# Kernel optimization log

Hardware: AMD Instinct MI355X
Metric: run time of the kernel (lower is better)

## Reference

```python
import jax, jax.numpy as jnp
import numpy as np

B, T, V = 2, 2048, 256
C, H, L = 1024, 16, 8
DH = C // H  # 64


def setup_inputs() -> dict:
    key = jax.random.key(0)
    ks = jax.random.split(key, 12)
    s = 0.02
    return {
        "x": jax.random.normal(ks[0], (B, T, V), jnp.float32),
        "W_emb": jax.random.normal(ks[1], (V, C), jnp.float32) * s,
        "b_emb": jnp.zeros((C,), jnp.float32),
        "pos": jax.random.normal(ks[2], (1, T, C), jnp.float32) * s,
        "Wqkv": jax.random.normal(ks[3], (L, C, 3 * C), jnp.float32) * s,
        "bqkv": jnp.zeros((L, 3 * C), jnp.float32),
        "Wproj": jax.random.normal(ks[4], (L, C, C), jnp.float32) * s,
        "bproj": jnp.zeros((L, C), jnp.float32),
        "gamma": jnp.ones((C,), jnp.float32),
        "beta": jnp.zeros((C,), jnp.float32),
        "W_out": jax.random.normal(ks[5], (C, V), jnp.float32) * s,
        "b_out": jnp.zeros((V,), jnp.float32),
    }


def _attn_block(h, Wqkv_l, bqkv_l, Wproj_l, bproj_l):
    # h: [B, T, C]
    qkv = h @ Wqkv_l + bqkv_l                      # [B, T, 3C]
    q, k, v = jnp.split(qkv, 3, axis=-1)
    q = q.reshape(B, T, H, DH)
    k = k.reshape(B, T, H, DH)
    v = v.reshape(B, T, H, DH)
    scale = 1.0 / np.sqrt(DH).astype(np.float32)
    att = jnp.einsum("bthd,bshd->bhts", q, k) * scale   # [B, H, T, T]
    att = jax.nn.softmax(att, axis=-1)
    y = jnp.einsum("bhts,bshd->bthd", att, v)            # [B, T, H, DH]
    y = y.reshape(B, T, C)
    return y @ Wproj_l + bproj_l


def reference(x, W_emb, b_emb, pos, Wqkv, bqkv, Wproj, bproj, gamma, beta, W_out, b_out):
    h = x @ W_emb + b_emb            # dense embedding: Linear(V -> C)
    h = h + pos[:, :T, :]
    # NOTE: original blocks return attention output directly (no residual, no MLP)
    def body(h, params):
        Wq, bq, Wp, bp = params
        return _attn_block(h, Wq, bq, Wp, bp), None
    h, _ = jax.lax.scan(body, h, (Wqkv, bqkv, Wproj, bproj))
    # LayerNorm
    mu = jnp.mean(h, axis=-1, keepdims=True)
    var = jnp.mean(jnp.square(h - mu), axis=-1, keepdims=True)
    h = (h - mu) * jax.lax.rsqrt(var + 1e-5) * gamma + beta
    return h @ W_out + b_out          # [B, T, V]
```

## Files before the change

kernel.cpp:

```cpp
#include <hip/hip_runtime.h>
#include <hip/hip_bf16.h>

#define T_SEQ 2048
#define BATCH 2
#define CDIM 1024
#define VDIM 256
#define NHEAD 16
#define DHEAD 64
#define NLAYER 8
#define MROWS (BATCH * T_SEQ)

typedef __attribute__((ext_vector_type(8))) short bf16x8;
typedef __attribute__((ext_vector_type(4))) float f32x4;
typedef __attribute__((ext_vector_type(4))) int i32x4;

#define SELHI 0x07060302u
#define SELLO 0x05040100u
#define QSCALE 0.18033688011112042f

__device__ __forceinline__ uint prm(uint a, uint b, uint s) { return __builtin_amdgcn_perm(a, b, s); }

__device__ __forceinline__ uint bf16rne(float f) {
    uint u = __float_as_uint(f);
    return (u + 0x7fffu + ((u >> 16) & 1u)) & 0xffff0000u;
}
__device__ __forceinline__ uint packsplit(float x) {
    uint hb = bf16rne(x);
    float d = x - __uint_as_float(hb);
    uint lb = bf16rne(d);
    return prm(hb, lb, SELHI);
}
__device__ __forceinline__ float unpack2(uint u) {
    return __uint_as_float(u & 0xffff0000u) + __uint_as_float(u << 16);
}
__device__ __forceinline__ bf16x8 asb(i32x4 v) {
    union { i32x4 i; bf16x8 b; } u; u.i = v; return u.b;
}
__device__ __forceinline__ short bfs(float f) { return (short)(bf16rne(f) >> 16); }


__global__ __launch_bounds__(256) void gemm_f32_kernel(
    const float* __restrict__ A, const float* __restrict__ B,
    const float* __restrict__ bias, const float* __restrict__ addrow,
    float* __restrict__ C, int M, int N, int K, int addmod, int out_mode)
{
    __shared__ float As[16][64];
    __shared__ float Bs[16][68];

    const int tid = threadIdx.x;
    const int bn = blockIdx.x * 64;
    const int bm = blockIdx.y * 64;

    const int lrow = tid >> 2;
    const int lkq  = (tid & 3) * 4;
    const int lkr  = tid >> 4;
    const int lnq  = (tid & 15) * 4;
    const int ty   = tid >> 4;
    const int tx   = tid & 15;

    float acc[4][4];
#pragma unroll
    for (int i = 0; i < 4; ++i)
#pragma unroll
        for (int j = 0; j < 4; ++j) acc[i][j] = 0.f;

    for (int k0 = 0; k0 < K; k0 += 16) {
        __syncthreads();
        {
            float4 a4 = *(const float4*)&A[(size_t)(bm + lrow) * K + k0 + lkq];
            As[lkq + 0][lrow] = a4.x;
            As[lkq + 1][lrow] = a4.y;
            As[lkq + 2][lrow] = a4.z;
            As[lkq + 3][lrow] = a4.w;
            *(float4*)&Bs[lkr][lnq] =
                *(const float4*)&B[(size_t)(k0 + lkr) * N + bn + lnq];
        }
        __syncthreads();
#pragma unroll
        for (int kk = 0; kk < 16; ++kk) {
            const float4 a = *(const float4*)&As[kk][ty * 4];
            const float4 b = *(const float4*)&Bs[kk][tx * 4];
            acc[0][0] += a.x * b.x; acc[0][1] += a.x * b.y; acc[0][2] += a.x * b.z; acc[0][3] += a.x * b.w;
            acc[1][0] += a.y * b.x; acc[1][1] += a.y * b.y; acc[1][2] += a.y * b.z; acc[1][3] += a.y * b.w;
            acc[2][0] += a.z * b.x; acc[2][1] += a.z * b.y; acc[2][2] += a.z * b.z; acc[2][3] += a.z * b.w;
            acc[3][0] += a.w * b.x; acc[3][1] += a.w * b.y; acc[3][2] += a.w * b.z; acc[3][3] += a.w * b.w;
        }
    }

    const int ncol = bn + tx * 4;
    const float4 bv = *(const float4*)&bias[ncol];
#pragma unroll
    for (int i = 0; i < 4; ++i) {
        const int mrow = bm + ty * 4 + i;
        float4 o;
        o.x = acc[i][0] + bv.x;
        o.y = acc[i][1] + bv.y;
        o.z = acc[i][2] + bv.z;
        o.w = acc[i][3] + bv.w;
        if (addrow) {
            const float4 p = *(const float4*)&addrow[(size_t)(mrow % addmod) * N + ncol];
            o.x += p.x; o.y += p.y; o.z += p.z; o.w += p.w;
        }
        if (out_mode == 0) {
            *(float4*)&C[(size_t)mrow * N + ncol] = o;
        } else {
            const size_t addr = ((size_t)(mrow >> 4) * (N >> 5) + (ncol >> 5)) * 512
                              + (size_t)(((ncol >> 2) & 3) * 16 + (mrow & 15)) * 8
                              + 4 * ((ncol >> 4) & 1);
            uint4 pk;
            pk.x = packsplit(o.x); pk.y = packsplit(o.y);
            pk.z = packsplit(o.z); pk.w = packsplit(o.w);
            *(uint4*)&((uint*)C)[addr] = pk;
        }
    }
}

__global__ __launch_bounds__(256) void wsplit_kernel(
    const float* __restrict__ W, short* __restrict__ Fh, short* __restrict__ Fl,
    int N, int K)
{
    const int ln = threadIdx.x & 63, lk = threadIdx.x >> 6;
    const int n  = blockIdx.x * 64 + ln;
    const int kq = blockIdx.y * 4 + lk;
    const int k0 = kq * 4;

    float f0 = W[(size_t)(k0 + 0) * N + n];
    float f1 = W[(size_t)(k0 + 1) * N + n];
    float f2 = W[(size_t)(k0 + 2) * N + n];
    float f3 = W[(size_t)(k0 + 3) * N + n];
    uint h0 = bf16rne(f0), h1 = bf16rne(f1), h2 = bf16rne(f2), h3 = bf16rne(f3);
    uint l0 = bf16rne(f0 - __uint_as_float(h0));
    uint l1 = bf16rne(f1 - __uint_as_float(h1));
    uint l2 = bf16rne(f2 - __uint_as_float(h2));
    uint l3 = bf16rne(f3 - __uint_as_float(h3));

    const int gl = kq & 3, j0 = ((kq >> 2) & 1) * 4;
    const size_t base = (((size_t)(n >> 4) * (K >> 5) + (kq >> 3)) * 64 + gl * 16 + (n & 15)) * 8 + j0;
    *(int2*)&Fh[base] = make_int2((int)prm(h1, h0, SELHI), (int)prm(h3, h2, SELHI));
    *(int2*)&Fl[base] = make_int2((int)prm(l1, l0, SELHI), (int)prm(l3, l2, SELHI));
}

template <int TERMS>
__global__ __launch_bounds__(256) void gemm_mfma_kernel(
    const uint* __restrict__ Apf, const short* __restrict__ Bhf,
    const short* __restrict__ Blf, const float* __restrict__ bias,
    uint* __restrict__ Cv, uint* __restrict__ Cq, short* __restrict__ Ckf,
    short* __restrict__ Cvf, int M, int N, int K, int out_mode)
{
    const int tid = threadIdx.x, lane = tid & 63, w = tid >> 6;
    const int wr = w >> 1, wc = w & 1, x = lane & 15, gl = lane >> 4;
    const int bm = blockIdx.y * 128, bn = blockIdx.x * 128;
    const int nkc = K >> 5;

    const uint*  ab = Apf + ((size_t)((bm >> 4) + wr * 4) * nkc) * 512 + (size_t)lane * 8;
    const short* hb = Bhf + (((size_t)((bn >> 4) + wc * 4) * nkc) * 64 + lane) * 8;
    const short* lb = Blf + (((size_t)((bn >> 4) + wc * 4) * nkc) * 64 + lane) * 8;
    const size_t tstr = (size_t)nkc * 512;

    f32x4 acc[4][4];
#pragma unroll
    for (int mi = 0; mi < 4; ++mi)
#pragma unroll
        for (int ni = 0; ni < 4; ++ni) acc[mi][ni] = (f32x4){0.f, 0.f, 0.f, 0.f};

    for (int kc = 0; kc < nkc; ++kc) {
        const size_t ko = (size_t)kc * 512;
        bf16x8 ah[4], al[4], bh[4], bl[4];
#pragma unroll
        for (int t = 0; t < 4; ++t) {
            const uint* ap = ab + t * tstr + ko;
            uint4 a0 = *(const uint4*)ap;
            uint4 a1 = *(const uint4*)(ap + 4);
            i32x4 h4;
            h4[0] = (int)prm(a0.y, a0.x, SELHI); h4[1] = (int)prm(a0.w, a0.z, SELHI);
            h4[2] = (int)prm(a1.y, a1.x, SELHI); h4[3] = (int)prm(a1.w, a1.z, SELHI);
            ah[t] = asb(h4);
            if (TERMS >= 2) {
                i32x4 l4;
                l4[0] = (int)prm(a0.y, a0.x, SELLO); l4[1] = (int)prm(a0.w, a0.z, SELLO);
                l4[2] = (int)prm(a1.y, a1.x, SELLO); l4[3] = (int)prm(a1.w, a1.z, SELLO);
                al[t] = asb(l4);
            }
            bh[t] = *(const bf16x8*)(hb + t * tstr + ko);
            if (TERMS >= 3) bl[t] = *(const bf16x8*)(lb + t * tstr + ko);
        }
        __builtin_amdgcn_s_setprio(1);
#pragma unroll
        for (int mi = 0; mi < 4; ++mi)
#pragma unroll
            for (int ni = 0; ni < 4; ++ni) {
                acc[mi][ni] = __builtin_amdgcn_mfma_f32_16x16x32_bf16(ah[mi], bh[ni], acc[mi][ni], 0, 0, 0);
                if (TERMS >= 3)
                    acc[mi][ni] = __builtin_amdgcn_mfma_f32_16x16x32_bf16(ah[mi], bl[ni], acc[mi][ni], 0, 0, 0);
                if (TERMS >= 2)
                    acc[mi][ni] = __builtin_amdgcn_mfma_f32_16x16x32_bf16(al[mi], bh[ni], acc[mi][ni], 0, 0, 0);
            }
        __builtin_amdgcn_s_setprio(0);
    }

#pragma unroll
    for (int ni = 0; ni < 4; ++ni) {
        const int n = bn + wc * 64 + ni * 16 + x;
        const float bv = bias[n];
#pragma unroll
        for (int mi = 0; mi < 4; ++mi) {
            const int m0 = bm + wr * 64 + mi * 16 + gl * 4;
            const f32x4 o = acc[mi][ni];
            if (out_mode == 2) {
                const size_t mt = (size_t)(bm >> 4) + wr * 4 + mi;
                const size_t base = (mt * (N >> 5) + (n >> 5)) * 512
                                  + (size_t)(((n >> 2) & 3) * 16 + gl * 4) * 8
                                  + (n & 3) + 4 * ((n >> 4) & 1);
                Cv[base + 0 * 8] = packsplit(o[0] + bv);
                Cv[base + 1 * 8] = packsplit(o[1] + bv);
                Cv[base + 2 * 8] = packsplit(o[2] + bv);
                Cv[base + 3 * 8] = packsplit(o[3] + bv);
            } else if (n < 1024) {
                Cq[(size_t)(m0 + 0) * 1024 + n] = packsplit((o[0] + bv) * QSCALE);
                Cq[(size_t)(m0 + 1) * 1024 + n] = packsplit((o[1] + bv) * QSCALE);
                Cq[(size_t)(m0 + 2) * 1024 + n] = packsplit((o[2] + bv) * QSCALE);
                Cq[(size_t)(m0 + 3) * 1024 + n] = packsplit((o[3] + bv) * QSCALE);
            } else if (n < 2048) {
                const int dd6 = n - 1024;
                const int hhh = dd6 >> 6, ch = (dd6 >> 5) & 1, dd = dd6 & 31;
                const int bq = m0 >> 11, sv = m0 & (T_SEQ - 1);
                const size_t base = ((((size_t)(bq * NHEAD + hhh) * 128 + (sv >> 4)) * 2 + ch) * 64
                                    + 16 * ((dd & 15) >> 2) + (sv & 15)) * 8
                                    + (dd & 3) + 4 * (dd >> 4);
                Ckf[base + 0]  = bfs(o[0] + bv);
                Ckf[base + 8]  = bfs(o[1] + bv);
                Ckf[base + 16] = bfs(o[2] + bv);
                Ckf[base + 24] = bfs(o[3] + bv);
            } else {
                const int dd6 = n - 2048;
                const int hhh = dd6 >> 6, dmi = (dd6 >> 4) & 3, xt = dd6 & 15;
                const int bq = m0 >> 11, sv = m0 & (T_SEQ - 1);
                const size_t base = ((((size_t)(bq * NHEAD + hhh) * 64 + (sv >> 5)) * 4 + dmi) * 64
                                    + xt + 16 * ((sv & 15) >> 2)) * 8 + 4 * ((sv >> 4) & 1);
                short4 st;
                st.x = bfs(o[0] + bv); st.y = bfs(o[1] + bv);
                st.z = bfs(o[2] + bv); st.w = bfs(o[3] + bv);
                *(short4*)&Cvf[base] = st;
            }
        }
    }
}

__global__ __launch_bounds__(256) void attn_mfma_kernel(
    const uint* __restrict__ qrow, const short* __restrict__ kf,
    const short* __restrict__ vf, uint* __restrict__ y)
{
    const int tid  = threadIdx.x;
    const int w    = tid >> 6;
    const int lane = tid & 63;
    const int x    = lane & 15;
    const int gl   = lane >> 4;

    const int orig = blockIdx.x;
    const int wgid = (orig & 7) * 64 + (orig >> 3);
    const int bh = wgid >> 4;
    const int b = bh >> 4, hh = bh & 15;
    const int t0 = (wgid & 15) * 128;

    i32x4 qhi[2][2];
#pragma unroll
    for (int qf = 0; qf < 2; ++qf) {
        const uint* qp = qrow + (size_t)(b * T_SEQ + t0 + 64 * qf + 16 * w + x) * 1024 + hh * 64;
#pragma unroll
        for (int ch = 0; ch < 2; ++ch) {
            uint4 a0 = *(const uint4*)(qp + 32 * ch + 4 * gl);
            uint4 a1 = *(const uint4*)(qp + 32 * ch + 16 + 4 * gl);
            qhi[qf][ch][0] = (int)prm(a0.y, a0.x, SELHI); qhi[qf][ch][1] = (int)prm(a0.w, a0.z, SELHI);
            qhi[qf][ch][2] = (int)prm(a1.y, a1.x, SELHI); qhi[qf][ch][3] = (int)prm(a1.w, a1.z, SELHI);
        }
    }

    const short* kb = kf + (size_t)bh * 128 * 2 * 512 + (size_t)lane * 8;
    const short* vb = vf + (size_t)bh * 64 * 4 * 512 + (size_t)lane * 8;

    i32x4 ones4;
    ones4[0] = ones4[1] = ones4[2] = ones4[3] = 0x3F803F80;

    f32x4 oacc[2][4], lacc[2];
#pragma unroll
    for (int qf = 0; qf < 2; ++qf) {
        lacc[qf] = (f32x4){0.f, 0.f, 0.f, 0.f};
#pragma unroll
        for (int i = 0; i < 4; ++i) oacc[qf][i] = (f32x4){0.f, 0.f, 0.f, 0.f};
    }

    for (int s0 = 0; s0 < T_SEQ; s0 += 64) {
        bf16x8 kh[4][2], vh[2][4];
#pragma unroll
        for (int sc = 0; sc < 4; ++sc)
#pragma unroll
            for (int ch = 0; ch < 2; ++ch)
                kh[sc][ch] = *(const bf16x8*)(kb + ((((size_t)(s0 >> 4) + sc) * 2 + ch) * 512));
#pragma unroll
        for (int ch = 0; ch < 2; ++ch)
#pragma unroll
            for (int dm = 0; dm < 4; ++dm)
                vh[ch][dm] = *(const bf16x8*)(vb + ((((size_t)(s0 >> 5) + ch) * 4 + dm) * 512));

#pragma unroll
        for (int qf = 0; qf < 2; ++qf) {
            f32x4 s4[4];
#pragma unroll
            for (int sc = 0; sc < 4; ++sc) {
                s4[sc] = (f32x4){0.f, 0.f, 0.f, 0.f};
                s4[sc] = __builtin_amdgcn_mfma_f32_16x16x32_bf16(kh[sc][0], asb(qhi[qf][0]), s4[sc], 0, 0, 0);
                s4[sc] = __builtin_amdgcn_mfma_f32_16x16x32_bf16(kh[sc][1], asb(qhi[qf][1]), s4[sc], 0, 0, 0);
            }
#pragma unroll
            for (int sc = 0; sc < 4; ++sc) {
                s4[sc][0] = __builtin_amdgcn_exp2f(s4[sc][0]);
                s4[sc][1] = __builtin_amdgcn_exp2f(s4[sc][1]);
                s4[sc][2] = __builtin_amdgcn_exp2f(s4[sc][2]);
                s4[sc][3] = __builtin_amdgcn_exp2f(s4[sc][3]);
            }
            i32x4 pfh[2];
#pragma unroll
            for (int c = 0; c < 2; ++c) {
                f32x4 pa = s4[2 * c], pb = s4[2 * c + 1];
                pfh[c][0] = (int)prm(__float_as_uint(pa[1]), __float_as_uint(pa[0]), SELHI);
                pfh[c][1] = (int)prm(__float_as_uint(pa[3]), __float_as_uint(pa[2]), SELHI);
                pfh[c][2] = (int)prm(__float_as_uint(pb[1]), __float_as_uint(pb[0]), SELHI);
                pfh[c][3] = (int)prm(__float_as_uint(pb[3]), __float_as_uint(pb[2]), SELHI);
            }
            lacc[qf] = __builtin_amdgcn_mfma_f32_16x16x32_bf16(asb(ones4), asb(pfh[0]), lacc[qf], 0, 0, 0);
            lacc[qf] = __builtin_amdgcn_mfma_f32_16x16x32_bf16(asb(ones4), asb(pfh[1]), lacc[qf], 0, 0, 0);
#pragma unroll
            for (int dm = 0; dm < 4; ++dm) {
                oacc[qf][dm] = __builtin_amdgcn_mfma_f32_16x16x32_bf16(vh[0][dm], asb(pfh[0]), oacc[qf][dm], 0, 0, 0);
                oacc[qf][dm] = __builtin_amdgcn_mfma_f32_16x16x32_bf16(vh[1][dm], asb(pfh[1]), oacc[qf][dm], 0, 0, 0);
            }
        }
    }

#pragma unroll
    for (int qf = 0; qf < 2; ++qf) {
        const float invl = 1.f / lacc[qf][0];
        const size_t mt = (size_t)((b * T_SEQ + t0) >> 4) + 4 * qf + w;
#pragma unroll
        for (int dm = 0; dm < 4; ++dm) {
            f32x4 o = oacc[qf][dm];
            const size_t addr = (mt * 32 + hh * 2 + (dm >> 1)) * 512
                              + (size_t)lane * 8 + 4 * (dm & 1);
            uint4 pk;
            pk.x = packsplit(o[0] * invl); pk.y = packsplit(o[1] * invl);
            pk.z = packsplit(o[2] * invl); pk.w = packsplit(o[3] * invl);
            *(uint4*)&y[addr] = pk;
        }
    }
}

__global__ __launch_bounds__(256) void ln_kernel(
    const uint* __restrict__ h, const float* __restrict__ gamma,
    const float* __restrict__ beta, float* __restrict__ out)
{
    const int row = blockIdx.x;
    const int tid = threadIdx.x;

    const size_t addr = ((size_t)(row >> 4) * 32 + (tid >> 3)) * 512
                      + (size_t)((tid & 3) * 16 + (row & 15)) * 8
                      + 4 * ((tid >> 2) & 1);
    uint4 u = *(const uint4*)&h[addr];
    float4 v;
    v.x = unpack2(u.x); v.y = unpack2(u.y); v.z = unpack2(u.z); v.w = unpack2(u.w);

    float s  = v.x + v.y + v.z + v.w;
    float ss = v.x * v.x + v.y * v.y + v.z * v.z + v.w * v.w;
#pragma unroll
    for (int off = 1; off < 64; off <<= 1) {
        s  += __shfl_xor(s, off);
        ss += __shfl_xor(ss, off);
    }
    __shared__ float rs[4], rss[4];
    const int wid = tid >> 6;
    if ((tid & 63) == 0) { rs[wid] = s; rss[wid] = ss; }
    __syncthreads();
    s  = rs[0] + rs[1] + rs[2] + rs[3];
    ss = rss[0] + rss[1] + rss[2] + rss[3];

    const float mu   = s * (1.f / (float)CDIM);
    const float var  = ss * (1.f / (float)CDIM) - mu * mu;
    const float rstd = rsqrtf(var + 1e-5f);

    const float4 g  = *(const float4*)&gamma[tid * 4];
    const float4 be = *(const float4*)&beta[tid * 4];
    float4 o;
    o.x = (v.x - mu) * rstd * g.x + be.x;
    o.y = (v.y - mu) * rstd * g.y + be.y;
    o.z = (v.z - mu) * rstd * g.z + be.z;
    o.w = (v.w - mu) * rstd * g.w + be.w;
    *(float4*)&out[(size_t)row * CDIM + tid * 4] = o;
}

extern "C" void kernel_launch(void* const* d_in, const int* in_sizes, int n_in,
                              void* d_out, int out_size, void* d_ws, size_t ws_size,
                              hipStream_t stream)
{
    const float* x      = (const float*)d_in[0];
    const float* W_emb  = (const float*)d_in[1];
    const float* b_emb  = (const float*)d_in[2];
    const float* pos    = (const float*)d_in[3];
    const float* Wqkv   = (const float*)d_in[4];
    const float* bqkv   = (const float*)d_in[5];
    const float* Wproj  = (const float*)d_in[6];
    const float* bproj  = (const float*)d_in[7];
    const float* gamma  = (const float*)d_in[8];
    const float* beta   = (const float*)d_in[9];
    const float* W_out  = (const float*)d_in[10];
    const float* b_out  = (const float*)d_in[11];
    float* out = (float*)d_out;

    uint* h    = (uint*)d_ws;
    uint* qrow = h + (size_t)MROWS * CDIM;
    uint* y    = qrow + (size_t)MROWS * CDIM;
    short* kf  = (short*)(y + (size_t)MROWS * CDIM);
    short* vfb = kf + (size_t)32 * 128 * 2 * 512;
    short* Bqh = vfb + (size_t)32 * 64 * 4 * 512;
    short* Bql = Bqh + (size_t)3 * CDIM * CDIM;
    short* Bph = Bql + (size_t)3 * CDIM * CDIM;
    short* Bpl = Bph + (size_t)CDIM * CDIM;

    const dim3 blk(256);
    const int nattn = (T_SEQ / 128) * BATCH * NHEAD;

    gemm_f32_kernel<<<dim3(CDIM / 64, MROWS / 64), blk, 0, stream>>>(
        x, W_emb, b_emb, pos, (float*)h, MROWS, CDIM, VDIM, T_SEQ, 2);
    for (int l = 0; l < NLAYER; ++l) {
        wsplit_kernel<<<dim3(3 * CDIM / 64, CDIM / 16), blk, 0, stream>>>(
            Wqkv + (size_t)l * CDIM * 3 * CDIM, Bqh, Bql, 3 * CDIM, CDIM);
        gemm_mfma_kernel<1><<<dim3(3 * CDIM / 128, MROWS / 128), blk, 0, stream>>>(
            h, Bqh, Bql, bqkv + (size_t)l * 3 * CDIM,
            nullptr, qrow, kf, vfb, MROWS, 3 * CDIM, CDIM, 3);
        attn_mfma_kernel<<<dim3(nattn), blk, 0, stream>>>(qrow, kf, vfb, y);
        wsplit_kernel<<<dim3(CDIM / 64, CDIM / 16), blk, 0, stream>>>(
            Wproj + (size_t)l * CDIM * CDIM, Bph, Bpl, CDIM, CDIM);
        gemm_mfma_kernel<3><<<dim3(CDIM / 128, MROWS / 128), blk, 0, stream>>>(
            y, Bph, Bpl, bproj + (size_t)l * CDIM,
            h, nullptr, nullptr, nullptr, MROWS, CDIM, CDIM, 2);
    }
    ln_kernel<<<dim3(MROWS), blk, 0, stream>>>(h, gamma, beta, (float*)y);
    gemm_f32_kernel<<<dim3(VDIM / 64, MROWS / 64), blk, 0, stream>>>(
        (float*)y, W_out, b_out, nullptr, out, MROWS, VDIM, CDIM, 1, 0);
}
```

Before: 1.191 ms.

## Move embedding and output projections onto split-bf16 MFMA GEMM path

Replaces the scalar fp32 GEMMs for the embedding and output projection with the split-bf16 MFMA GEMM. It adds packing kernels for x and the weights, fuses the positional add into the GEMM epilogue and makes LayerNorm emit the packed split format. It also skips computing and writing the unused low-part of Wqkv, since the QKV GEMM only uses one term. This adds extra pack/split launches and relies on the three-term bf16 split to keep fp32-level accuracy.

```diff
diff --git a/kernel.cpp b/kernel.cpp
--- a/kernel.cpp
+++ b/kernel.cpp
@@ -39,80 +39,20 @@
 __device__ __forceinline__ short bfs(float f) { return (short)(bf16rne(f) >> 16); }
 
 
-__global__ __launch_bounds__(256) void gemm_f32_kernel(
-    const float* __restrict__ A, const float* __restrict__ B,
-    const float* __restrict__ bias, const float* __restrict__ addrow,
-    float* __restrict__ C, int M, int N, int K, int addmod, int out_mode)
-{
-    __shared__ float As[16][64];
-    __shared__ float Bs[16][68];
-
-    const int tid = threadIdx.x;
-    const int bn = blockIdx.x * 64;
-    const int bm = blockIdx.y * 64;
-
-    const int lrow = tid >> 2;
-    const int lkq  = (tid & 3) * 4;
-    const int lkr  = tid >> 4;
-    const int lnq  = (tid & 15) * 4;
-    const int ty   = tid >> 4;
-    const int tx   = tid & 15;
-
-    float acc[4][4];
-#pragma unroll
-    for (int i = 0; i < 4; ++i)
-#pragma unroll
-        for (int j = 0; j < 4; ++j) acc[i][j] = 0.f;
-
-    for (int k0 = 0; k0 < K; k0 += 16) {
-        __syncthreads();
-        {
-            float4 a4 = *(const float4*)&A[(size_t)(bm + lrow) * K + k0 + lkq];
-            As[lkq + 0][lrow] = a4.x;
-            As[lkq + 1][lrow] = a4.y;
-            As[lkq + 2][lrow] = a4.z;
-            As[lkq + 3][lrow] = a4.w;
-            *(float4*)&Bs[lkr][lnq] =
-                *(const float4*)&B[(size_t)(k0 + lkr) * N + bn + lnq];
-        }
-        __syncthreads();
-#pragma unroll
-        for (int kk = 0; kk < 16; ++kk) {
-            const float4 a = *(const float4*)&As[kk][ty * 4];
-            const float4 b = *(const float4*)&Bs[kk][tx * 4];
-            acc[0][0] += a.x * b.x; acc[0][1] += a.x * b.y; acc[0][2] += a.x * b.z; acc[0][3] += a.x * b.w;
-            acc[1][0] += a.y * b.x; acc[1][1] += a.y * b.y; acc[1][2] += a.y * b.z; acc[1][3] += a.y * b.w;
-            acc[2][0] += a.z * b.x; acc[2][1] += a.z * b.y; acc[2][2] += a.z * b.z; acc[2][3] += a.z * b.w;
-            acc[3][0] += a.w * b.x; acc[3][1] += a.w * b.y; acc[3][2] += a.w * b.z; acc[3][3] += a.w * b.w;
-        }
-    }
-
-    const int ncol = bn + tx * 4;
-    const float4 bv = *(const float4*)&bias[ncol];
-#pragma unroll
-    for (int i = 0; i < 4; ++i) {
-        const int mrow = bm + ty * 4 + i;
-        float4 o;
-        o.x = acc[i][0] + bv.x;
-        o.y = acc[i][1] + bv.y;
-        o.z = acc[i][2] + bv.z;
-        o.w = acc[i][3] + bv.w;
-        if (addrow) {
-            const float4 p = *(const float4*)&addrow[(size_t)(mrow % addmod) * N + ncol];
-            o.x += p.x; o.y += p.y; o.z += p.z; o.w += p.w;
-        }
-        if (out_mode == 0) {
-            *(float4*)&C[(size_t)mrow * N + ncol] = o;
-        } else {
-            const size_t addr = ((size_t)(mrow >> 4) * (N >> 5) + (ncol >> 5)) * 512
-                              + (size_t)(((ncol >> 2) & 3) * 16 + (mrow & 15)) * 8
-                              + 4 * ((ncol >> 4) & 1);
-            uint4 pk;
-            pk.x = packsplit(o.x); pk.y = packsplit(o.y);
-            pk.z = packsplit(o.z); pk.w = packsplit(o.w);
-            *(uint4*)&((uint*)C)[addr] = pk;
-        }
-    }
+__global__ __launch_bounds__(256) void packx_kernel(
+    const float* __restrict__ x, uint* __restrict__ xpf)
+{
+    const int t  = blockIdx.x * 256 + threadIdx.x;
+    const int m  = t >> 6;
+    const int k0 = (t & 63) * 4;
+    const float4 v = *(const float4*)&x[(size_t)m * 256 + k0];
+    const size_t addr = ((size_t)(m >> 4) * 8 + (k0 >> 5)) * 512
+                      + (size_t)(((k0 >> 2) & 3) * 16 + (m & 15)) * 8
+                      + 4 * ((k0 >> 4) & 1);
+    uint4 pk;
+    pk.x = packsplit(v.x); pk.y = packsplit(v.y);
+    pk.z = packsplit(v.z); pk.w = packsplit(v.w);
+    *(uint4*)&xpf[addr] = pk;
 }
 
 __global__ __launch_bounds__(256) void wsplit_kernel(
@@ -129,21 +69,24 @@
     float f2 = W[(size_t)(k0 + 2) * N + n];
     float f3 = W[(size_t)(k0 + 3) * N + n];
     uint h0 = bf16rne(f0), h1 = bf16rne(f1), h2 = bf16rne(f2), h3 = bf16rne(f3);
-    uint l0 = bf16rne(f0 - __uint_as_float(h0));
-    uint l1 = bf16rne(f1 - __uint_as_float(h1));
-    uint l2 = bf16rne(f2 - __uint_as_float(h2));
-    uint l3 = bf16rne(f3 - __uint_as_float(h3));
 
     const int gl = kq & 3, j0 = ((kq >> 2) & 1) * 4;
     const size_t base = (((size_t)(n >> 4) * (K >> 5) + (kq >> 3)) * 64 + gl * 16 + (n & 15)) * 8 + j0;
     *(int2*)&Fh[base] = make_int2((int)prm(h1, h0, SELHI), (int)prm(h3, h2, SELHI));
-    *(int2*)&Fl[base] = make_int2((int)prm(l1, l0, SELHI), (int)prm(l3, l2, SELHI));
+    if (Fl) {
+        uint l0 = bf16rne(f0 - __uint_as_float(h0));
+        uint l1 = bf16rne(f1 - __uint_as_float(h1));
+        uint l2 = bf16rne(f2 - __uint_as_float(h2));
+        uint l3 = bf16rne(f3 - __uint_as_float(h3));
+        *(int2*)&Fl[base] = make_int2((int)prm(l1, l0, SELHI), (int)prm(l3, l2, SELHI));
+    }
 }
 
 template <int TERMS>
 __global__ __launch_bounds__(256) void gemm_mfma_kernel(
     const uint* __restrict__ Apf, const short* __restrict__ Bhf,
     const short* __restrict__ Blf, const float* __restrict__ bias,
+    const float* __restrict__ addrow,
     uint* __restrict__ Cv, uint* __restrict__ Cq, short* __restrict__ Ckf,
     short* __restrict__ Cvf, int M, int N, int K, int out_mode)
 {
@@ -206,15 +149,28 @@
         for (int mi = 0; mi < 4; ++mi) {
             const int m0 = bm + wr * 64 + mi * 16 + gl * 4;
             const f32x4 o = acc[mi][ni];
-            if (out_mode == 2) {
+            if (out_mode == 0) {
+                float* C = (float*)Cv;
+                C[(size_t)(m0 + 0) * N + n] = o[0] + bv;
+                C[(size_t)(m0 + 1) * N + n] = o[1] + bv;
+                C[(size_t)(m0 + 2) * N + n] = o[2] + bv;
+                C[(size_t)(m0 + 3) * N + n] = o[3] + bv;
+            } else if (out_mode == 2) {
+                float p0 = 0.f, p1 = 0.f, p2 = 0.f, p3 = 0.f;
+                if (addrow) {
+                    p0 = addrow[(size_t)((m0 + 0) & (T_SEQ - 1)) * N + n];
+                    p1 = addrow[(size_t)((m0 + 1) & (T_SEQ - 1)) * N + n];
+                    p2 = addrow[(size_t)((m0 + 2) & (T_SEQ - 1)) * N + n];
+                    p3 = addrow[(size_t)((m0 + 3) & (T_SEQ - 1)) * N + n];
+                }
                 const size_t mt = (size_t)(bm >> 4) + wr * 4 + mi;
                 const size_t base = (mt * (N >> 5) + (n >> 5)) * 512
                                   + (size_t)(((n >> 2) & 3) * 16 + gl * 4) * 8
                                   + (n & 3) + 4 * ((n >> 4) & 1);
-                Cv[base + 0 * 8] = packsplit(o[0] + bv);
-                Cv[base + 1 * 8] = packsplit(o[1] + bv);
-                Cv[base + 2 * 8] = packsplit(o[2] + bv);
-                Cv[base + 3 * 8] = packsplit(o[3] + bv);
+                Cv[base + 0 * 8] = packsplit(o[0] + bv + p0);
+                Cv[base + 1 * 8] = packsplit(o[1] + bv + p1);
+                Cv[base + 2 * 8] = packsplit(o[2] + bv + p2);
+                Cv[base + 3 * 8] = packsplit(o[3] + bv + p3);
             } else if (n < 1024) {
                 Cq[(size_t)(m0 + 0) * 1024 + n] = packsplit((o[0] + bv) * QSCALE);
                 Cq[(size_t)(m0 + 1) * 1024 + n] = packsplit((o[1] + bv) * QSCALE);
@@ -356,7 +312,7 @@
 
 __global__ __launch_bounds__(256) void ln_kernel(
     const uint* __restrict__ h, const float* __restrict__ gamma,
-    const float* __restrict__ beta, float* __restrict__ out)
+    const float* __restrict__ beta, uint* __restrict__ outp)
 {
     const int row = blockIdx.x;
     const int tid = threadIdx.x;
@@ -388,12 +344,12 @@
 
     const float4 g  = *(const float4*)&gamma[tid * 4];
     const float4 be = *(const float4*)&beta[tid * 4];
-    float4 o;
-    o.x = (v.x - mu) * rstd * g.x + be.x;
-    o.y = (v.y - mu) * rstd * g.y + be.y;
-    o.z = (v.z - mu) * rstd * g.z + be.z;
-    o.w = (v.w - mu) * rstd * g.w + be.w;
-    *(float4*)&out[(size_t)row * CDIM + tid * 4] = o;
+    uint4 pk;
+    pk.x = packsplit((v.x - mu) * rstd * g.x + be.x);
+    pk.y = packsplit((v.y - mu) * rstd * g.y + be.y);
+    pk.z = packsplit((v.z - mu) * rstd * g.z + be.z);
+    pk.w = packsplit((v.w - mu) * rstd * g.w + be.w);
+    *(uint4*)&outp[addr] = pk;
 }
 
 extern "C" void kernel_launch(void* const* d_in, const int* in_sizes, int n_in,
@@ -423,26 +379,36 @@
     short* Bql = Bqh + (size_t)3 * CDIM * CDIM;
     short* Bph = Bql + (size_t)3 * CDIM * CDIM;
     short* Bpl = Bph + (size_t)CDIM * CDIM;
+    short* Eh  = Bpl + (size_t)CDIM * CDIM;
+    short* El  = Eh  + (size_t)VDIM * CDIM;
+    short* Oh  = El  + (size_t)VDIM * CDIM;
+    short* Ol  = Oh  + (size_t)CDIM * VDIM;
+    uint*  xpf = (uint*)(Ol + (size_t)CDIM * VDIM);
 
     const dim3 blk(256);
     const int nattn = (T_SEQ / 128) * BATCH * NHEAD;
 
-    gemm_f32_kernel<<<dim3(CDIM / 64, MROWS / 64), blk, 0, stream>>>(
-        x, W_emb, b_emb, pos, (float*)h, MROWS, CDIM, VDIM, T_SEQ, 2);
+    packx_kernel<<<dim3(MROWS * (VDIM / 4) / 256), blk, 0, stream>>>(x, xpf);
+    wsplit_kernel<<<dim3(CDIM / 64, VDIM / 16), blk, 0, stream>>>(W_emb, Eh, El, CDIM, VDIM);
+    gemm_mfma_kernel<3><<<dim3(CDIM / 128, MROWS / 128), blk, 0, stream>>>(
+        xpf, Eh, El, b_emb, pos, h, nullptr, nullptr, nullptr, MROWS, CDIM, VDIM, 2);
+
     for (int l = 0; l < NLAYER; ++l) {
         wsplit_kernel<<<dim3(3 * CDIM / 64, CDIM / 16), blk, 0, stream>>>(
-            Wqkv + (size_t)l * CDIM * 3 * CDIM, Bqh, Bql, 3 * CDIM, CDIM);
+            Wqkv + (size_t)l * CDIM * 3 * CDIM, Bqh, nullptr, 3 * CDIM, CDIM);
         gemm_mfma_kernel<1><<<dim3(3 * CDIM / 128, MROWS / 128), blk, 0, stream>>>(
-            h, Bqh, Bql, bqkv + (size_t)l * 3 * CDIM,
+            h, Bqh, nullptr, bqkv + (size_t)l * 3 * CDIM, nullptr,
             nullptr, qrow, kf, vfb, MROWS, 3 * CDIM, CDIM, 3);
         attn_mfma_kernel<<<dim3(nattn), blk, 0, stream>>>(qrow, kf, vfb, y);
         wsplit_kernel<<<dim3(CDIM / 64, CDIM / 16), blk, 0, stream>>>(
             Wproj + (size_t)l * CDIM * CDIM, Bph, Bpl, CDIM, CDIM);
         gemm_mfma_kernel<3><<<dim3(CDIM / 128, MROWS / 128), blk, 0, stream>>>(
-            y, Bph, Bpl, bproj + (size_t)l * CDIM,
+            y, Bph, Bpl, bproj + (size_t)l * CDIM, nullptr,
             h, nullptr, nullptr, nullptr, MROWS, CDIM, CDIM, 2);
     }
-    ln_kernel<<<dim3(MROWS), blk, 0, stream>>>(h, gamma, beta, (float*)y);
-    gemm_f32_kernel<<<dim3(VDIM / 64, MROWS / 64), blk, 0, stream>>>(
-        (float*)y, W_out, b_out, nullptr, out, MROWS, VDIM, CDIM, 1, 0);
-}
+
+    ln_kernel<<<dim3(MROWS), blk, 0, stream>>>(h, gamma, beta, y);
+    wsplit_kernel<<<dim3(VDIM / 64, CDIM / 16), blk, 0, stream>>>(W_out, Oh, Ol, VDIM, CDIM);
+    gemm_mfma_kernel<3><<<dim3(VDIM / 128, MROWS / 128), blk, 0, stream>>>(
+        y, Oh, Ol, b_out, nullptr, (uint*)out, nullptr, nullptr, nullptr, MROWS, VDIM, CDIM, 0);
+}
```

After: 1.162 ms. -2.4%, faster.
